# Kernel optimization log

Measured on AMD Instinct MI355X. Metric: run time of the kernel, lower is better.

The kernel has to match this reference:

```python
import jax, jax.numpy as jnp
import numpy as np

BLOCK = 128  # fp8 block-quant block size (128, 128)


def dequant_block_fp8_weight(w, scale_inv):
    """w: [O, I] fp8-valued weights (stored as f32); scale_inv: [O//128, I//128].
    Dequant = per-(128,128)-block multiply by scale."""
    O, I = w.shape
    wb = w.reshape(O // BLOCK, BLOCK, I // BLOCK, BLOCK)
    wb = wb * scale_inv[:, None, :, None]
    return wb.reshape(O, I)


def setup_inputs() -> dict:
    key = jax.random.key(0)
    ks = jax.random.split(key, 7)
    H, F, T = 5120, 1536, 8192  # hidden, moe_intermediate, tokens
    x = jax.random.normal(ks[0], (T, H), dtype=jnp.float32)
    w_gate = jax.random.normal(ks[1], (F, H), dtype=jnp.float32)
    s_gate = jax.random.uniform(ks[2], (F // BLOCK, H // BLOCK), dtype=jnp.float32) * 0.01 + 1e-4
    w_up = jax.random.normal(ks[3], (F, H), dtype=jnp.float32)
    s_up = jax.random.uniform(ks[4], (F // BLOCK, H // BLOCK), dtype=jnp.float32) * 0.01 + 1e-4
    w_down = jax.random.normal(ks[5], (H, F), dtype=jnp.float32)
    s_down = jax.random.uniform(ks[6], (H // BLOCK, F // BLOCK), dtype=jnp.float32) * 0.01 + 1e-4
    return {"x": x, "w_gate": w_gate, "s_gate": s_gate, "w_up": w_up,
            "s_up": s_up, "w_down": w_down, "s_down": s_down}


def reference(x, w_gate, s_gate, w_up, s_up, w_down, s_down):
    # down_proj(silu(gate_proj(x)) * up_proj(x)), each Linear dequantizing
    # block-scaled fp8 weights first (bias=False everywhere).
    wg = dequant_block_fp8_weight(w_gate, s_gate).astype(x.dtype)
    wu = dequant_block_fp8_weight(w_up, s_up).astype(x.dtype)
    wd = dequant_block_fp8_weight(w_down, s_down).astype(x.dtype)
    gate = jnp.einsum('th,fh->tf', x, wg)  # [T, F]
    up = jnp.einsum('th,fh->tf', x, wu)    # [T, F]
    h = jax.nn.silu(gate) * up
    out = jnp.einsum('tf,hf->th', h, wd)   # [T, H]
    return out
```

## Files before the change

kernel.cpp:

```cpp
#include <hip/hip_runtime.h>


typedef __bf16 bf16x8 __attribute__((ext_vector_type(8)));
typedef float  f32x4  __attribute__((ext_vector_type(4)));

__device__ __forceinline__ void glds16(const __bf16* g, __bf16* l) {
  __builtin_amdgcn_global_load_lds(
      (const __attribute__((address_space(1))) void*)g,
      (__attribute__((address_space(3))) void*)l, 16, 0, 0);
}

__device__ __forceinline__ void chunk_rk(int c, int& row, int& k) {
  int s = c >> 6;
  int w = (c & 63) << 4;
  int wl = w ^ (((w >> 9) & 1) << 5) ^ (((w >> 7) & 1) << 4);
  row = (s << 4) + (wl >> 6);
  k = (wl & 63) >> 1;
}

#define SYNC(n)                                                        \
  do {                                                                 \
    __builtin_amdgcn_sched_barrier(0);                                 \
    asm volatile("s_waitcnt vmcnt(" #n ")\n\ts_barrier" ::: "memory"); \
    __builtin_amdgcn_sched_barrier(0);                                 \
  } while (0)

__device__ __forceinline__ void cast8(const float* __restrict__ in,
                                      __bf16* __restrict__ out, size_t idx) {
  f32x4 a = *(const f32x4*)(in + idx);
  f32x4 b = *(const f32x4*)(in + idx + 4);
  bf16x8 o;
#pragma unroll
  for (int i = 0; i < 4; ++i) { o[i] = (__bf16)a[i]; o[i + 4] = (__bf16)b[i]; }
  *(bf16x8*)(out + idx) = o;
}

__device__ __forceinline__ void dq_ilv(const float* __restrict__ w,
                                       const float* __restrict__ s,
                                       __bf16* __restrict__ wq, int r, int tid,
                                       int which) {
  unsigned idx = ((unsigned)r * 256u + (unsigned)tid) * 8u;
  unsigned f = idx / 5120u;
  unsigned h = idx - f * 5120u;
  float sc = s[(f >> 7) * 40 + (h >> 7)];
  f32x4 a = *(const f32x4*)(w + idx);
  f32x4 b = *(const f32x4*)(w + idx + 4);
  bf16x8 o;
#pragma unroll
  for (int i = 0; i < 4; ++i) {
    o[i] = (__bf16)(a[i] * sc);
    o[i + 4] = (__bf16)(b[i] * sc);
  }
  *(bf16x8*)(wq + (size_t)(2 * f + which) * 5120 + h) = o;
}

__device__ __forceinline__ void dq_wd(const float* __restrict__ w,
                                      const float* __restrict__ s,
                                      __bf16* __restrict__ o8, int r, int tid) {
  unsigned idx = ((unsigned)r * 256u + (unsigned)tid) * 8u;
  unsigned f = idx / 1536u;
  unsigned h = idx - f * 1536u;
  float sc = s[(f >> 7) * 12 + (h >> 7)];
  f32x4 a = *(const f32x4*)(w + idx);
  f32x4 b = *(const f32x4*)(w + idx + 4);
  bf16x8 o;
#pragma unroll
  for (int i = 0; i < 4; ++i) {
    o[i] = (__bf16)(a[i] * sc);
    o[i + 4] = (__bf16)(b[i] * sc);
  }
  *(bf16x8*)(o8 + idx) = o;
}

__global__ void prep(const float* __restrict__ x, const float* __restrict__ wg,
                     const float* __restrict__ sg, const float* __restrict__ wu,
                     const float* __restrict__ su, const float* __restrict__ wd,
                     const float* __restrict__ sd, __bf16* __restrict__ xb,
                     __bf16* __restrict__ wq, __bf16* __restrict__ wdq) {
  int bid = blockIdx.x;
  int tid = threadIdx.x;
  if (bid < 20480) {
    cast8(x, xb, ((size_t)bid * 256 + tid) * 8);
  } else if (bid < 24320) {
    dq_ilv(wg, sg, wq, bid - 20480, tid, 0);
  } else if (bid < 28160) {
    dq_ilv(wu, su, wq, bid - 24320, tid, 1);
  } else {
    dq_wd(wd, sd, wdq, bid - 28160, tid);
  }
}

template <bool FUSE_SILU, typename OutT>
__global__ __launch_bounds__(512, 2) void gemm_p(
    const __bf16* __restrict__ A, const __bf16* __restrict__ B,
    OutT* __restrict__ C, int M, int N, int K, int ldc, int nbx) {
  __shared__ __bf16 lds[4 * 12288];
  const int tid = threadIdx.x;
  const int lane = tid & 63;
  const int wave = tid >> 6;
  const int lr = lane & 15;

  const int nwg = gridDim.x;
  const int lb = (blockIdx.x & 7) * (nwg >> 3) + (blockIdx.x >> 3);
  const int bx = lb % nbx;
  const int by = lb / nbx;
  const int m0 = by * 128, n0 = bx * 256;

  int laneoff = (lr << 6) | ((lane >> 4) << 4);
  laneoff ^= ((lr & 2) << 3) | ((lr & 8) << 2);
  const int wm4 = wave & 4;
  const int wn4 = (wave & 3) << 2;

  int ra, ka, rb0, kb0, rb1, kb1;
  chunk_rk(tid, ra, ka);
  chunk_rk(tid, rb0, kb0);
  chunk_rk(tid + 512, rb1, kb1);
  const __bf16* Ab = A + (size_t)m0 * K;
  const __bf16* Bb = B + (size_t)n0 * K;
  const unsigned offA = (unsigned)ra * K + (unsigned)ka;
  const unsigned offB0 = (unsigned)rb0 * K + (unsigned)kb0;
  const unsigned offB1 = (unsigned)rb1 * K + (unsigned)kb1;

  f32x4 acc[4][4] = {};

  auto STAGE = [&](int t, int bufi) {
    __bf16* lb_ = lds + bufi * 12288;
    const unsigned ko = (unsigned)t << 5;
    glds16(Ab + (offA + ko), lb_ + (tid << 3));
    glds16(Bb + (offB0 + ko), lb_ + 4096 + (tid << 3));
    glds16(Bb + (offB1 + ko), lb_ + 4096 + ((tid + 512) << 3));
  };
  auto COMPUTE = [&](int bufi) {
    const char* base = (const char*)lds + bufi * 24576;
    bf16x8 af[4], bg[4];
#pragma unroll
    for (int i = 0; i < 4; ++i)
      af[i] = *(const bf16x8*)(base + ((wm4 + i) << 10) + laneoff);
#pragma unroll
    for (int j = 0; j < 4; ++j)
      bg[j] = *(const bf16x8*)(base + 8192 + ((wn4 + j) << 10) + laneoff);
    __builtin_amdgcn_s_setprio(1);
#pragma unroll
    for (int j = 0; j < 4; ++j)
#pragma unroll
      for (int i = 0; i < 4; ++i)
        acc[i][j] = __builtin_amdgcn_mfma_f32_16x16x32_bf16(af[i], bg[j],
                                                            acc[i][j], 0, 0, 0);
    __builtin_amdgcn_s_setprio(0);
  };

  const int NT = K >> 5;
  STAGE(0, 0);
  STAGE(1, 1);
  STAGE(2, 2);
  SYNC(6);
  int cur = 0;
  for (int t = 0; t < NT - 3; ++t) {
    STAGE(t + 3, (cur + 3) & 3);
    COMPUTE(cur);
    SYNC(6);
    cur = (cur + 1) & 3;
  }
  COMPUTE(cur); SYNC(3); cur = (cur + 1) & 3;
  COMPUTE(cur); SYNC(0); cur = (cur + 1) & 3;
  COMPUTE(cur);

  const int colb = n0 + (wn4 << 4) + lr;
  const int rowb = m0 + (wm4 << 4) + ((lane >> 4) << 2);
#pragma unroll
  for (int i = 0; i < 4; ++i)
#pragma unroll
    for (int j = 0; j < 4; ++j)
#pragma unroll
      for (int r = 0; r < 4; ++r) {
        if constexpr (FUSE_SILU) {
          float v = acc[i][j][r];
          float p = __shfl_xor(v, 1, 64);
          float g = (lane & 1) ? p : v;
          float u = (lane & 1) ? v : p;
          float hv = (g / (1.0f + __expf(-g))) * u;
          if ((lane & 1) == 0)
            C[(size_t)(rowb + i * 16 + r) * ldc + ((colb + j * 16) >> 1)] =
                (OutT)hv;
        } else {
          C[(size_t)(rowb + i * 16 + r) * ldc + (colb + j * 16)] =
              (OutT)acc[i][j][r];
        }
      }
}

extern "C" void kernel_launch(void* const* d_in, const int* in_sizes, int n_in,
                              void* d_out, int out_size, void* d_ws,
                              size_t ws_size, hipStream_t stream) {
  const int Hd = 5120, Fd = 1536, Td = 8192;
  const float* x = (const float*)d_in[0];
  const float* wg = (const float*)d_in[1];
  const float* sg = (const float*)d_in[2];
  const float* wu = (const float*)d_in[3];
  const float* su = (const float*)d_in[4];
  const float* wd = (const float*)d_in[5];
  const float* sd = (const float*)d_in[6];
  float* out = (float*)d_out;

  __bf16* ws = (__bf16*)d_ws;
  const size_t xsz = (size_t)Td * Hd;
  __bf16* xb = ws;
  __bf16* wq = xb + xsz;
  __bf16* wdq = wq + (size_t)2 * Fd * Hd;
  __bf16* hbuf = wdq + (size_t)Hd * Fd;

  prep<<<32000, 256, 0, stream>>>(x, wg, sg, wu, su, wd, sd, xb, wq, wdq);

  gemm_p<true, __bf16><<<768, 512, 0, stream>>>(xb, wq, hbuf, Td, 2 * Fd, Hd,
                                                Fd, 12);

  gemm_p<false, float><<<1280, 512, 0, stream>>>(hbuf, wdq, out, Td, Hd, Fd,
                                                 Hd, 20);
}
```

Baseline: 792.7 us.

## Prelayout weights in MFMA fragment order and load B directly to registers

The prep kernel now writes dequantized gate/up and down weights in a fragment-major layout matching the MFMA B operand per wave and k-step. The GEMM drops B from LDS, uses 256 threads with 4 waves each covering 128x64 outputs, and loads B fragments straight into registers with inline global_load_dwordx4, double-buffered across k-steps. Only A is staged through LDS (4 buffers), with reads split into halves interleaved with MFMAs. This cuts LDS traffic and footprint, at the cost of more accumulator registers per thread and uncoalesced-looking direct global loads whose latency must be hidden by the prefetch distance.

Result: faster. 698.3 us (-11.9%).

```diff
diff --git a/kernel.cpp b/kernel.cpp
--- a/kernel.cpp
+++ b/kernel.cpp
@@ -3,6 +3,7 @@
 
 typedef __bf16 bf16x8 __attribute__((ext_vector_type(8)));
 typedef float  f32x4  __attribute__((ext_vector_type(4)));
+typedef unsigned int u32x4 __attribute__((ext_vector_type(4)));
 
 __device__ __forceinline__ void glds16(const __bf16* g, __bf16* l) {
   __builtin_amdgcn_global_load_lds(
@@ -18,7 +19,13 @@
   k = (wl & 63) >> 1;
 }
 
-#define SYNC(n)                                                        \
+#define LGKM0()                                        \
+  do {                                                 \
+    asm volatile("s_waitcnt lgkmcnt(0)" ::: "memory"); \
+    __builtin_amdgcn_sched_barrier(0);                 \
+  } while (0)
+
+#define VMBAR(n)                                                       \
   do {                                                                 \
     __builtin_amdgcn_sched_barrier(0);                                 \
     asm volatile("s_waitcnt vmcnt(" #n ")\n\ts_barrier" ::: "memory"); \
@@ -33,43 +40,6 @@
 #pragma unroll
   for (int i = 0; i < 4; ++i) { o[i] = (__bf16)a[i]; o[i + 4] = (__bf16)b[i]; }
   *(bf16x8*)(out + idx) = o;
-}
-
-__device__ __forceinline__ void dq_ilv(const float* __restrict__ w,
-                                       const float* __restrict__ s,
-                                       __bf16* __restrict__ wq, int r, int tid,
-                                       int which) {
-  unsigned idx = ((unsigned)r * 256u + (unsigned)tid) * 8u;
-  unsigned f = idx / 5120u;
-  unsigned h = idx - f * 5120u;
-  float sc = s[(f >> 7) * 40 + (h >> 7)];
-  f32x4 a = *(const f32x4*)(w + idx);
-  f32x4 b = *(const f32x4*)(w + idx + 4);
-  bf16x8 o;
-#pragma unroll
-  for (int i = 0; i < 4; ++i) {
-    o[i] = (__bf16)(a[i] * sc);
-    o[i + 4] = (__bf16)(b[i] * sc);
-  }
-  *(bf16x8*)(wq + (size_t)(2 * f + which) * 5120 + h) = o;
-}
-
-__device__ __forceinline__ void dq_wd(const float* __restrict__ w,
-                                      const float* __restrict__ s,
-                                      __bf16* __restrict__ o8, int r, int tid) {
-  unsigned idx = ((unsigned)r * 256u + (unsigned)tid) * 8u;
-  unsigned f = idx / 1536u;
-  unsigned h = idx - f * 1536u;
-  float sc = s[(f >> 7) * 12 + (h >> 7)];
-  f32x4 a = *(const f32x4*)(w + idx);
-  f32x4 b = *(const f32x4*)(w + idx + 4);
-  bf16x8 o;
-#pragma unroll
-  for (int i = 0; i < 4; ++i) {
-    o[i] = (__bf16)(a[i] * sc);
-    o[i + 4] = (__bf16)(b[i] * sc);
-  }
-  *(bf16x8*)(o8 + idx) = o;
 }
 
 __global__ void prep(const float* __restrict__ x, const float* __restrict__ wg,
@@ -81,24 +51,62 @@
   int tid = threadIdx.x;
   if (bid < 20480) {
     cast8(x, xb, ((size_t)bid * 256 + tid) * 8);
-  } else if (bid < 24320) {
-    dq_ilv(wg, sg, wq, bid - 20480, tid, 0);
   } else if (bid < 28160) {
-    dq_ilv(wu, su, wq, bid - 24320, tid, 1);
+    unsigned g = (unsigned)(bid - 20480) * 256u + (unsigned)tid;
+    unsigned lane = g & 63u, c = lane & 15u, q = lane >> 4;
+    unsigned fr = (g >> 6) & 15u;
+    unsigned u = g >> 10;
+    unsigned bx = u / 160u;
+    unsigned t = u - bx * 160u;
+    unsigned nc = (bx << 8) | (fr << 4) | c;
+    unsigned k = (t << 5) | (q << 3);
+    unsigned f = nc >> 1;
+    const float* wsrc = (nc & 1) ? wu : wg;
+    const float* ssrc = (nc & 1) ? su : sg;
+    float sc = ssrc[(f >> 7) * 40 + (k >> 7)];
+    size_t si = (size_t)f * 5120 + k;
+    f32x4 a = *(const f32x4*)(wsrc + si);
+    f32x4 b = *(const f32x4*)(wsrc + si + 4);
+    bf16x8 o;
+#pragma unroll
+    for (int i = 0; i < 4; ++i) {
+      o[i] = (__bf16)(a[i] * sc);
+      o[i + 4] = (__bf16)(b[i] * sc);
+    }
+    *(bf16x8*)(wq + (size_t)g * 8) = o;
   } else {
-    dq_wd(wd, sd, wdq, bid - 28160, tid);
+    unsigned g = (unsigned)(bid - 28160) * 256u + (unsigned)tid;
+    unsigned lane = g & 63u, c = lane & 15u, q = lane >> 4;
+    unsigned fr = (g >> 6) & 15u;
+    unsigned u = g >> 10;
+    unsigned bx = u / 48u;
+    unsigned t = u - bx * 48u;
+    unsigned nc = (bx << 8) | (fr << 4) | c;
+    unsigned k = (t << 5) | (q << 3);
+    float sc = sd[(nc >> 7) * 12 + (k >> 7)];
+    size_t si = (size_t)nc * 1536 + k;
+    f32x4 a = *(const f32x4*)(wd + si);
+    f32x4 b = *(const f32x4*)(wd + si + 4);
+    bf16x8 o;
+#pragma unroll
+    for (int i = 0; i < 4; ++i) {
+      o[i] = (__bf16)(a[i] * sc);
+      o[i + 4] = (__bf16)(b[i] * sc);
+    }
+    *(bf16x8*)(wdq + (size_t)g * 8) = o;
   }
 }
 
 template <bool FUSE_SILU, typename OutT>
-__global__ __launch_bounds__(512, 2) void gemm_p(
-    const __bf16* __restrict__ A, const __bf16* __restrict__ B,
+__global__ __launch_bounds__(256, 2) void gemm_p(
+    const __bf16* __restrict__ A, const __bf16* __restrict__ Bfm,
     OutT* __restrict__ C, int M, int N, int K, int ldc, int nbx) {
-  __shared__ __bf16 lds[4 * 12288];
+  __shared__ __bf16 lds[4 * 4096];
   const int tid = threadIdx.x;
   const int lane = tid & 63;
   const int wave = tid >> 6;
   const int lr = lane & 15;
+  const int NT = K >> 5, NTm1 = NT - 1;
 
   const int nwg = gridDim.x;
   const int lb = (blockIdx.x & 7) * (nwg >> 3) + (blockIdx.x >> 3);
@@ -108,67 +116,92 @@
 
   int laneoff = (lr << 6) | ((lane >> 4) << 4);
   laneoff ^= ((lr & 2) << 3) | ((lr & 8) << 2);
-  const int wm4 = wave & 4;
-  const int wn4 = (wave & 3) << 2;
-
-  int ra, ka, rb0, kb0, rb1, kb1;
-  chunk_rk(tid, ra, ka);
-  chunk_rk(tid, rb0, kb0);
-  chunk_rk(tid + 512, rb1, kb1);
+
+  int r0, k0, r1, k1;
+  chunk_rk(tid, r0, k0);
+  chunk_rk(tid + 256, r1, k1);
+  const unsigned o0 = (unsigned)r0 * K + (unsigned)k0;
+  const unsigned o1 = (unsigned)r1 * K + (unsigned)k1;
+  const int d0 = tid << 3, d1 = (tid + 256) << 3;
   const __bf16* Ab = A + (size_t)m0 * K;
-  const __bf16* Bb = B + (size_t)n0 * K;
-  const unsigned offA = (unsigned)ra * K + (unsigned)ka;
-  const unsigned offB0 = (unsigned)rb0 * K + (unsigned)kb0;
-  const unsigned offB1 = (unsigned)rb1 * K + (unsigned)kb1;
-
-  f32x4 acc[4][4] = {};
-
-  auto STAGE = [&](int t, int bufi) {
-    __bf16* lb_ = lds + bufi * 12288;
-    const unsigned ko = (unsigned)t << 5;
-    glds16(Ab + (offA + ko), lb_ + (tid << 3));
-    glds16(Bb + (offB0 + ko), lb_ + 4096 + (tid << 3));
-    glds16(Bb + (offB1 + ko), lb_ + 4096 + ((tid + 512) << 3));
+  const __bf16* Bf =
+      Bfm + ((size_t)bx * NT * 16 + wave * 4) * 512 + (size_t)lane * 8;
+
+  f32x4 acc[8][4] = {};
+  bf16x8 af[4];
+  u32x4 bgA[4], bgB[4];
+
+  auto STAGE_A = [&](int t_, int s_) {
+    __bf16* lp = lds + s_ * 4096;
+    const unsigned ko = (unsigned)t_ << 5;
+    glds16(Ab + (o0 + ko), lp + d0);
+    glds16(Ab + (o1 + ko), lp + d1);
   };
-  auto COMPUTE = [&](int bufi) {
-    const char* base = (const char*)lds + bufi * 24576;
-    bf16x8 af[4], bg[4];
+  auto RD_A = [&](const char* cb, int h) {
 #pragma unroll
     for (int i = 0; i < 4; ++i)
-      af[i] = *(const bf16x8*)(base + ((wm4 + i) << 10) + laneoff);
-#pragma unroll
-    for (int j = 0; j < 4; ++j)
-      bg[j] = *(const bf16x8*)(base + 8192 + ((wn4 + j) << 10) + laneoff);
+      af[i] = *(const bf16x8*)(cb + (((h << 2) + i) << 10) + laneoff);
+  };
+  auto MFMA16 = [&](int h, u32x4 (&bk)[4]) {
     __builtin_amdgcn_s_setprio(1);
 #pragma unroll
-    for (int j = 0; j < 4; ++j)
+    for (int j = 0; j < 4; ++j) {
+      bf16x8 b = __builtin_bit_cast(bf16x8, bk[j]);
 #pragma unroll
       for (int i = 0; i < 4; ++i)
-        acc[i][j] = __builtin_amdgcn_mfma_f32_16x16x32_bf16(af[i], bg[j],
-                                                            acc[i][j], 0, 0, 0);
+        acc[(h << 2) + i][j] = __builtin_amdgcn_mfma_f32_16x16x32_bf16(
+            af[i], b, acc[(h << 2) + i][j], 0, 0, 0);
+    }
     __builtin_amdgcn_s_setprio(0);
   };
 
-  const int NT = K >> 5;
-  STAGE(0, 0);
-  STAGE(1, 1);
-  STAGE(2, 2);
-  SYNC(6);
-  int cur = 0;
-  for (int t = 0; t < NT - 3; ++t) {
-    STAGE(t + 3, (cur + 3) & 3);
-    COMPUTE(cur);
-    SYNC(6);
-    cur = (cur + 1) & 3;
-  }
-  COMPUTE(cur); SYNC(3); cur = (cur + 1) & 3;
-  COMPUTE(cur); SYNC(0); cur = (cur + 1) & 3;
-  COMPUTE(cur);
-
-  const int colb = n0 + (wn4 << 4) + lr;
-  const int rowb = m0 + (wm4 << 4) + ((lane >> 4) << 2);
-#pragma unroll
-  for (int i = 0; i < 4; ++i)
+#define B_LOAD(t_, B_)                                                       \
+  {                                                                          \
+    const __bf16* bp = Bf + (size_t)(t_) * 8192;                             \
+    asm volatile("global_load_dwordx4 %0, %1, off" : "=v"(B_[0]) : "v"(bp)); \
+    asm volatile("global_load_dwordx4 %0, %1, off offset:1024"               \
+                 : "=v"(B_[1]) : "v"(bp));                                   \
+    asm volatile("global_load_dwordx4 %0, %1, off offset:2048"               \
+                 : "=v"(B_[2]) : "v"(bp));                                   \
+    asm volatile("global_load_dwordx4 %0, %1, off offset:3072"               \
+                 : "=v"(B_[3]) : "v"(bp));                                   \
+  }
+
+  STAGE_A(0, 0);
+  B_LOAD(0, bgA);
+  STAGE_A(1, 1);
+  B_LOAD(1, bgB);
+
+#define KSTEP(u_, B_)                                \
+  {                                                  \
+    int tn = t + (u_) + 2;                           \
+    if (tn > NTm1) tn = NTm1;      \
+    const char* cb = (const char*)lds + (u_) * 8192; \
+    VMBAR(6);                                        \
+    RD_A(cb, 0);                                     \
+    STAGE_A(tn, ((u_) + 2) & 3);                     \
+    LGKM0();                                         \
+    MFMA16(0, B_);                                   \
+    RD_A(cb, 1);                                     \
+    LGKM0();                                         \
+    MFMA16(1, B_);                                   \
+    B_LOAD(tn, B_);                                  \
+  }
+
+  for (int t = 0; t < NT; t += 4) {
+    KSTEP(0, bgA);
+    KSTEP(1, bgB);
+    KSTEP(2, bgA);
+    KSTEP(3, bgB);
+  }
+  VMBAR(0);
+#undef KSTEP
+#undef B_LOAD
+
+  const int colb = n0 + (wave << 6) + lr;
+  const int rowb = m0 + ((lane >> 4) << 2);
+#pragma unroll
+  for (int i = 0; i < 8; ++i)
 #pragma unroll
     for (int j = 0; j < 4; ++j)
 #pragma unroll
@@ -205,15 +238,15 @@
   __bf16* ws = (__bf16*)d_ws;
   const size_t xsz = (size_t)Td * Hd;
   __bf16* xb = ws;
-  __bf16* wq = xb + xsz;
-  __bf16* wdq = wq + (size_t)2 * Fd * Hd;
-  __bf16* hbuf = wdq + (size_t)Hd * Fd;
-
-  prep<<<32000, 256, 0, stream>>>(x, wg, sg, wu, su, wd, sd, xb, wq, wdq);
-
-  gemm_p<true, __bf16><<<768, 512, 0, stream>>>(xb, wq, hbuf, Td, 2 * Fd, Hd,
+  __bf16* wqf = xb + xsz;
+  __bf16* wdqf = wqf + (size_t)2 * Fd * Hd;
+  __bf16* hbuf = wdqf + (size_t)Hd * Fd;
+
+  prep<<<32000, 256, 0, stream>>>(x, wg, sg, wu, su, wd, sd, xb, wqf, wdqf);
+
+  gemm_p<true, __bf16><<<768, 256, 0, stream>>>(xb, wqf, hbuf, Td, 2 * Fd, Hd,
                                                 Fd, 12);
 
-  gemm_p<false, float><<<1280, 512, 0, stream>>>(hbuf, wdq, out, Td, Hd, Fd,
+  gemm_p<false, float><<<1280, 256, 0, stream>>>(hbuf, wdqf, out, Td, Hd, Fd,
                                                  Hd, 20);
 }
```
